# Kernel tuning notes

Measured on AMD Instinct MI355X. Metric: run time of the kernel, lower is better.

The kernel has to match this reference:

```python
import jax, jax.numpy as jnp
import numpy as np

EPS = 1e-3  # matches module default eps=0.001


def setup_inputs() -> dict:
    key = jax.random.key(0)
    k1, k2 = jax.random.split(key)
    B, C, W, H = 8, 64, 496, 432  # KITTI BEV grid, pillar feature dim 64
    x = jax.random.normal(k1, (B, C, W, H), dtype=jnp.float32)
    # are exactly zero across all channels so x.sum(1) == 0 there.
    occ = (jax.random.uniform(k2, (B, W, H)) < 0.10).astype(jnp.float32)
    x = x * occ[:, None, :, :]
    return {"x": x}


def reference(x):
    # Faithful to the torch module, including its padding artifact: each batch's
    # nonzero index list is padded to N = max(num_nonzeros) with index (0,0), so
    # padded slots gather x[b,:,0,0], contribute to mean/var with multiplicity
    # (N - n_b), and scatter a normalized value back into pixel (0,0).
    B, C, Wd, Hd = x.shape
    mask = (x.sum(axis=1) != 0)                 # [B,W,H] occupied pixels
    n = mask.sum(axis=(1, 2))                    # [B] nonzeros per batch
    N = n.max()                                  # padded gather length
    pad = (N - n).astype(x.dtype)                # [B] number of (0,0) pad slots
    x00 = x[:, :, 0, 0]                          # [B,C] value gathered by pads
    mb = mask[:, None, :, :].astype(x.dtype)     # [B,1,W,H]

    count = (B * N).astype(x.dtype)              # total gathered entries
    total = (x * mb).sum(axis=(0, 2, 3)) + (pad[:, None] * x00).sum(axis=0)  # [C]
    mean = total / count                         # [C]

    d = x - mean[None, :, None, None]
    sq = ((d * d) * mb).sum(axis=(0, 2, 3)) + (pad[:, None] * (x00 - mean) ** 2).sum(axis=0)
    var = sq / count                             # [C] biased variance (mean over gathered)

    inv = 1.0 / jnp.sqrt(var + EPS)              # [C]; note: mean is NOT subtracted
    out = jnp.where(mask[:, None, :, :], x * inv[None, :, None, None], x)

    # scatter-back hits (0,0) whenever batch b had pad slots OR (0,0) was nonzero
    write00 = (pad > 0) | mask[:, 0, 0]          # [B]
    out = out.at[:, :, 0, 0].set(
        jnp.where(write00[:, None], x00 * inv[None, :], out[:, :, 0, 0])
    )
    return out
```

## Files before the change

kernel.cpp:

```cpp
#include <hip/hip_runtime.h>

#define WH      214272
#define GPB     53568
#define NPLANE  512
#define NGROUP  (8*GPB)

#define STATS_BLOCKS 856

__global__ __launch_bounds__(256) void k_stats(const float4* __restrict__ x4,
                                               float* __restrict__ gsum,
                                               float* __restrict__ gsq,
                                               int* __restrict__ gn) {
    const int tid  = threadIdx.x;
    const int lane = tid & 63;
    const int wave = tid >> 6;
    const int c0   = wave * 16;

    float acc[16];
    float acc2[16];
#pragma unroll
    for (int j = 0; j < 16; ++j) { acc[j] = 0.f; acc2[j] = 0.f; }

    const int stride = STATS_BLOCKS * 64;
    for (int i = blockIdx.x * 64 + lane; i < NGROUP; i += stride) {
        const int b = i / GPB;
        const int r = i - b * GPB;
        const float4* p = x4 + (size_t)(b * 64 + c0) * GPB + r;
        float sx = 0.f, sy = 0.f, sz = 0.f, sw = 0.f;
#pragma unroll
        for (int j = 0; j < 16; ++j) {
            const float4 v = p[(size_t)j * GPB];
            sx += v.x; sy += v.y; sz += v.z; sw += v.w;
            acc[j] += (v.x + v.y) + (v.z + v.w);
            acc2[j] = fmaf(v.w, v.w, fmaf(v.z, v.z, fmaf(v.y, v.y, fmaf(v.x, v.x, acc2[j]))));
        }
        if (wave == 0) {
            int cnt = (sx != 0.f) + (sy != 0.f) + (sz != 0.f) + (sw != 0.f);
#pragma unroll
            for (int m = 1; m < 64; m <<= 1) cnt += __shfl_xor(cnt, m, 64);
            if (lane == 0) atomicAdd(&gn[b], cnt);
        }
    }

    float mysum = 0.f, mysq = 0.f;
#pragma unroll
    for (int j = 0; j < 16; ++j) {
        float r1 = acc[j], r2 = acc2[j];
#pragma unroll
        for (int m = 1; m < 64; m <<= 1) {
            r1 += __shfl_xor(r1, m, 64);
            r2 += __shfl_xor(r2, m, 64);
        }
        if (lane == j) { mysum = r1; mysq = r2; }
    }
    if (lane < 16) {
        atomicAdd(&gsum[c0 + lane], mysum);
        atomicAdd(&gsq[c0 + lane], mysq);
    }
}

__global__ void k_finalize(const float* __restrict__ x,
                           const float* __restrict__ gsum,
                           const float* __restrict__ gsq,
                           const int* __restrict__ gn,
                           float* __restrict__ ginv) {
    const int c = threadIdx.x;
    int nb[8];
    int N = 0;
#pragma unroll
    for (int b = 0; b < 8; ++b) { nb[b] = gn[b]; N = max(N, nb[b]); }
    float total = gsum[c];
    float S2    = gsq[c];
#pragma unroll
    for (int b = 0; b < 8; ++b) {
        const float pad = (float)(N - nb[b]);
        const float x00 = x[(size_t)(b * 64 + c) * WH];
        total = fmaf(pad, x00, total);
        S2    = fmaf(pad, x00 * x00, S2);
    }
    const float count = (float)(8 * N);
    const float mean  = total / count;
    const float var   = S2 / count - mean * mean;
    ginv[c] = 1.0f / sqrtf(var + 0.001f);
}

__global__ __launch_bounds__(256) void k_scale(const float4* __restrict__ x4,
                                               float4* __restrict__ out4,
                                               const float* __restrict__ ginv) {
    const int p = blockIdx.x * 256 + threadIdx.x;
    if (p >= GPB) return;
    const int plane = blockIdx.y;
    const float inv = ginv[plane & 63];
    const size_t idx = (size_t)plane * GPB + p;
    float4 v = x4[idx];
    v.x *= inv; v.y *= inv; v.z *= inv; v.w *= inv;
    out4[idx] = v;
}

extern "C" void kernel_launch(void* const* d_in, const int* in_sizes, int n_in,
                              void* d_out, int out_size, void* d_ws, size_t ws_size,
                              hipStream_t stream) {
    const float* x  = (const float*)d_in[0];
    float* out      = (float*)d_out;
    float* wsf      = (float*)d_ws;
    float* gsum     = wsf;
    float* gsq      = wsf + 64;
    int*   gn       = (int*)(wsf + 128);
    float* ginv     = wsf + 136;

    hipMemsetAsync(d_ws, 0, 136 * sizeof(float), stream);

    k_stats<<<STATS_BLOCKS, 256, 0, stream>>>((const float4*)x, gsum, gsq, gn);
    k_finalize<<<1, 64, 0, stream>>>(x, gsum, gsq, gn, ginv);
    k_scale<<<dim3((GPB + 255) / 256, NPLANE), 256, 0, stream>>>(
        (const float4*)x, (float4*)out, ginv);
}
```

Measured before the change: 795.2 us.

## Fuse finalize into scale kernel with grid-stride loop and nontemporal stores

Removes the separate single-block finalize launch by having each block of the scale kernel recompute the per-channel inverse std into shared memory. The scale kernel becomes a persistent grid-stride loop over all float4 elements with nontemporal stores, and the stats kernel gets more blocks plus occupancy launch bounds and an unsigned division. This trades one kernel launch and its serialization gap for redundant finalize work in every block and a per-element integer division.

```diff
diff --git a/kernel.cpp b/kernel.cpp
--- a/kernel.cpp
+++ b/kernel.cpp
@@ -2,15 +2,18 @@
 
 #define WH      214272
 #define GPB     53568
-#define NPLANE  512
 #define NGROUP  (8*GPB)
+#define TOTAL4  (512*GPB)
 
-#define STATS_BLOCKS 856
+#define STATS_BLOCKS 1024
+#define SCALE_BLOCKS 2048
 
-__global__ __launch_bounds__(256) void k_stats(const float4* __restrict__ x4,
-                                               float* __restrict__ gsum,
-                                               float* __restrict__ gsq,
-                                               int* __restrict__ gn) {
+typedef float floatx4 __attribute__((ext_vector_type(4)));
+
+__global__ __launch_bounds__(256, 4) void k_stats(const floatx4* __restrict__ x4,
+                                                  float* __restrict__ gsum,
+                                                  float* __restrict__ gsq,
+                                                  int* __restrict__ gn) {
     const int tid  = threadIdx.x;
     const int lane = tid & 63;
     const int wave = tid >> 6;
@@ -23,13 +26,13 @@
 
     const int stride = STATS_BLOCKS * 64;
     for (int i = blockIdx.x * 64 + lane; i < NGROUP; i += stride) {
-        const int b = i / GPB;
+        const int b = (int)((unsigned)i / GPB);
         const int r = i - b * GPB;
-        const float4* p = x4 + (size_t)(b * 64 + c0) * GPB + r;
+        const floatx4* p = x4 + (size_t)(b * 64 + c0) * GPB + r;
         float sx = 0.f, sy = 0.f, sz = 0.f, sw = 0.f;
 #pragma unroll
         for (int j = 0; j < 16; ++j) {
-            const float4 v = p[(size_t)j * GPB];
+            const floatx4 v = p[(size_t)j * GPB];
             sx += v.x; sy += v.y; sz += v.z; sw += v.w;
             acc[j] += (v.x + v.y) + (v.z + v.w);
             acc2[j] = fmaf(v.w, v.w, fmaf(v.z, v.z, fmaf(v.y, v.y, fmaf(v.x, v.x, acc2[j]))));
@@ -59,42 +62,44 @@
     }
 }
 
-__global__ void k_finalize(const float* __restrict__ x,
-                           const float* __restrict__ gsum,
-                           const float* __restrict__ gsq,
-                           const int* __restrict__ gn,
-                           float* __restrict__ ginv) {
-    const int c = threadIdx.x;
-    int nb[8];
-    int N = 0;
+__global__ __launch_bounds__(256, 8) void k_scale(const floatx4* __restrict__ x4,
+                                                  floatx4* __restrict__ out4,
+                                                  const float* __restrict__ gsum,
+                                                  const float* __restrict__ gsq,
+                                                  const int* __restrict__ gn) {
+    __shared__ float sinv[64];
+    const int tid = threadIdx.x;
+    if (tid < 64) {
+        const int c = tid;
+        const float* x = (const float*)x4;
+        int nb[8];
+        int N = 0;
 #pragma unroll
-    for (int b = 0; b < 8; ++b) { nb[b] = gn[b]; N = max(N, nb[b]); }
-    float total = gsum[c];
-    float S2    = gsq[c];
+        for (int b = 0; b < 8; ++b) { nb[b] = gn[b]; N = max(N, nb[b]); }
+        float total = gsum[c];
+        float S2    = gsq[c];
 #pragma unroll
-    for (int b = 0; b < 8; ++b) {
-        const float pad = (float)(N - nb[b]);
-        const float x00 = x[(size_t)(b * 64 + c) * WH];
-        total = fmaf(pad, x00, total);
-        S2    = fmaf(pad, x00 * x00, S2);
+        for (int b = 0; b < 8; ++b) {
+            const float pad = (float)(N - nb[b]);
+            const float x00 = x[(size_t)(b * 64 + c) * WH];
+            total = fmaf(pad, x00, total);
+            S2    = fmaf(pad, x00 * x00, S2);
+        }
+        const float count = (float)(8 * N);
+        const float mean  = total / count;
+        const float var   = S2 / count - mean * mean;
+        sinv[c] = 1.0f / sqrtf(var + 0.001f);
     }
-    const float count = (float)(8 * N);
-    const float mean  = total / count;
-    const float var   = S2 / count - mean * mean;
-    ginv[c] = 1.0f / sqrtf(var + 0.001f);
-}
+    __syncthreads();
 
-__global__ __launch_bounds__(256) void k_scale(const float4* __restrict__ x4,
-                                               float4* __restrict__ out4,
-                                               const float* __restrict__ ginv) {
-    const int p = blockIdx.x * 256 + threadIdx.x;
-    if (p >= GPB) return;
-    const int plane = blockIdx.y;
-    const float inv = ginv[plane & 63];
-    const size_t idx = (size_t)plane * GPB + p;
-    float4 v = x4[idx];
-    v.x *= inv; v.y *= inv; v.z *= inv; v.w *= inv;
-    out4[idx] = v;
+    const int nthreads = SCALE_BLOCKS * 256;
+    for (int i = blockIdx.x * 256 + tid; i < TOTAL4; i += nthreads) {
+        const int plane = (int)((unsigned)i / GPB);
+        const float inv = sinv[plane & 63];
+        floatx4 v = x4[i];
+        v.x *= inv; v.y *= inv; v.z *= inv; v.w *= inv;
+        __builtin_nontemporal_store(v, &out4[i]);
+    }
 }
 
 extern "C" void kernel_launch(void* const* d_in, const int* in_sizes, int n_in,
@@ -106,12 +111,10 @@
     float* gsum     = wsf;
     float* gsq      = wsf + 64;
     int*   gn       = (int*)(wsf + 128);
-    float* ginv     = wsf + 136;
 
-    hipMemsetAsync(d_ws, 0, 136 * sizeof(float), stream);
+    (void)hipMemsetAsync(d_ws, 0, 136 * sizeof(float), stream);
 
-    k_stats<<<STATS_BLOCKS, 256, 0, stream>>>((const float4*)x, gsum, gsq, gn);
-    k_finalize<<<1, 64, 0, stream>>>(x, gsum, gsq, gn, ginv);
-    k_scale<<<dim3((GPB + 255) / 256, NPLANE), 256, 0, stream>>>(
-        (const float4*)x, (float4*)out, ginv);
+    k_stats<<<STATS_BLOCKS, 256, 0, stream>>>((const floatx4*)x, gsum, gsq, gn);
+    k_scale<<<SCALE_BLOCKS, 256, 0, stream>>>((const floatx4*)x, (floatx4*)out,
+                                              gsum, gsq, gn);
 }
```

New measurement: 796.4 us. About the same (+0.2%).
